# Kernel optimization log

Measured on AMD Instinct MI355X. Metric: run time of the kernel, lower is better.

## Reference

```python
import jax, jax.numpy as jnp
import numpy as np

N, D_IN, D_OUT, E = 8192, 2048, 2048, 8


def setup_inputs() -> dict:
    key = jax.random.key(0)
    k0, k1, k2, k3, k4, k5 = jax.random.split(key, 6)
    s = 1.0 / np.sqrt(D_IN)  # torch nn.Linear default init range
    return {
        "inputs": jax.random.normal(k0, (N, D_IN), jnp.float32),
        "condition": jax.random.normal(k1, (N, D_IN), jnp.float32),
        "Wp": jax.random.uniform(k2, (E, D_IN), jnp.float32, -s, s),
        "bp": jax.random.uniform(k3, (E,), jnp.float32, -s, s),
        "We": jax.random.uniform(k4, (E, D_OUT, D_IN), jnp.float32, -s, s),
        "be": jax.random.uniform(k5, (E, D_OUT), jnp.float32, -s, s),
    }


def reference(inputs, condition, Wp, bp, We, be):
    # predictor: gating logits [N, E]
    prediction = condition @ Wp.T + bp
    # straight-through multiplier: value == 1, gradient flows to prediction
    multiply = jnp.ones_like(prediction) + (prediction - jax.lax.stop_gradient(prediction))
    # run ALL experts on the full batch (faithful to the original): [E, N, F]
    expert_out = jnp.einsum('nd,efd->enf', inputs, We) + be[:, None, :]
    combined = multiply.T[:, :, None] * expert_out  # [E, N, F]
    # select the argmax expert per row
    idx = jnp.argmax(prediction, axis=-1)  # [N]
    result = combined[idx, jnp.arange(prediction.shape[0])]  # [N, F]
    return result
```

## Files before the change

### kernel.cpp

```cpp
#include <hip/hip_runtime.h>
#include <hip/hip_bf16.h>
#include <stdint.h>

#define N_ROWS 8192
#define DIN 2048
#define DOUT 2048
#define NE 8

#define BM3 320
#define BN3 256
#define BK2 64
#define RT3 33
#define NBLK3 (8 * RT3)

#define BM 128
#define BN 128
#define BK 64
#define MAX_RT 71

typedef __bf16 bf16x8 __attribute__((ext_vector_type(8)));
typedef float f32x4 __attribute__((ext_vector_type(4)));

__device__ __forceinline__ uint32_t f2bf(float f) {
  uint32_t u = __builtin_bit_cast(uint32_t, f);
  uint32_t r = u + 0x7FFFu + ((u >> 16) & 1u);
  return r >> 16;
}

__device__ __forceinline__ void gl2lds16(const void* g, void* l) {
  __builtin_amdgcn_global_load_lds(
      (const __attribute__((address_space(1))) unsigned int*)g,
      (__attribute__((address_space(3))) unsigned int*)l, 16, 0, 0);
}

__global__ __launch_bounds__(256) void gate_kernel(
    const float* __restrict__ cond, const float* __restrict__ Wp,
    const float* __restrict__ bp, const float* __restrict__ X,
    int* __restrict__ idx, int* __restrict__ counts, __hip_bfloat16* __restrict__ Xb)
{
  __shared__ int lc[NE];
  const int t = threadIdx.x;
  if (t < NE) lc[t] = 0;

  const int lane = t & 63;
  const int wid  = t >> 6;
  const int row  = blockIdx.x * 4 + wid;

  double acc[NE];
  #pragma unroll
  for (int e = 0; e < NE; ++e) acc[e] = 0.0;

  const float4* crow = (const float4*)(cond + (size_t)row * DIN);
  const float4* wp4  = (const float4*)Wp;
  #pragma unroll
  for (int i = 0; i < DIN / 256; ++i) {
    float4 c = crow[i * 64 + lane];
    #pragma unroll
    for (int e = 0; e < NE; ++e) {
      float4 w = wp4[e * (DIN / 4) + i * 64 + lane];
      acc[e] += (double)c.x * w.x + (double)c.y * w.y
              + (double)c.z * w.z + (double)c.w * w.w;
    }
  }
  #pragma unroll
  for (int e = 0; e < NE; ++e) {
    double v = acc[e];
    #pragma unroll
    for (int off = 32; off > 0; off >>= 1) v += __shfl_down(v, off, 64);
    acc[e] = v;
  }
  __syncthreads();
  if (lane == 0) {
    int best = 0; double bv = acc[0] + (double)bp[0];
    #pragma unroll
    for (int e = 1; e < NE; ++e) {
      double v = acc[e] + (double)bp[e];
      if (v > bv) { bv = v; best = e; }
    }
    idx[row] = best;
    atomicAdd(&lc[best], 1);
  }

  {
    const float4* xs = (const float4*)(X + (size_t)blockIdx.x * 4 * DIN);
    uint4* xd = (uint4*)(Xb + (size_t)blockIdx.x * 4 * DIN);
    #pragma unroll
    for (int c = 0; c < 4; ++c) {
      int ch = t + c * 256;
      float4 v0 = xs[ch * 2];
      float4 v1 = xs[ch * 2 + 1];
      uint4 o;
      o.x = f2bf(v0.x) | (f2bf(v0.y) << 16);
      o.y = f2bf(v0.z) | (f2bf(v0.w) << 16);
      o.z = f2bf(v1.x) | (f2bf(v1.y) << 16);
      o.w = f2bf(v1.z) | (f2bf(v1.w) << 16);
      xd[ch] = o;
    }
  }

  __syncthreads();
  if (t < NE && lc[t] > 0) atomicAdd(&counts[t], lc[t]);
}

__global__ void scan_kernel(const int* __restrict__ counts, int* __restrict__ offsets) {
  if (threadIdx.x == 0 && blockIdx.x == 0) {
    int s = 0;
    for (int e = 0; e < NE; ++e) { offsets[e] = s; s += counts[e]; }
  }
}

__global__ __launch_bounds__(256) void scatter_kernel(
    const int* __restrict__ idx, const int* __restrict__ offsets,
    int* __restrict__ fill, int* __restrict__ rows)
{
  __shared__ int lc[NE], lb[NE];
  const int t = threadIdx.x;
  if (t < NE) lc[t] = 0;
  __syncthreads();
  int n = blockIdx.x * 256 + t;
  int e = idx[n];
  int my = atomicAdd(&lc[e], 1);
  __syncthreads();
  if (t < NE) lb[t] = (lc[t] > 0) ? atomicAdd(&fill[t], lc[t]) : 0;
  __syncthreads();
  rows[offsets[e] + lb[e] + my] = n;
}

__global__ __launch_bounds__(256) void conv_kernel(
    const float* __restrict__ src, __hip_bfloat16* __restrict__ dst, size_t nchunks)
{
  const size_t stride = (size_t)gridDim.x * 256;
  for (size_t c = (size_t)blockIdx.x * 256 + threadIdx.x; c < nchunks; c += stride) {
    float4 v0 = ((const float4*)src)[c * 2];
    float4 v1 = ((const float4*)src)[c * 2 + 1];
    uint4 o;
    o.x = f2bf(v0.x) | (f2bf(v0.y) << 16);
    o.y = f2bf(v0.z) | (f2bf(v0.w) << 16);
    o.z = f2bf(v1.x) | (f2bf(v1.y) << 16);
    o.w = f2bf(v1.z) | (f2bf(v1.w) << 16);
    ((uint4*)dst)[c] = o;
  }
}

__global__ __launch_bounds__(512, 1) void moe_gemm8(
    const __hip_bfloat16* __restrict__ Xb, const __hip_bfloat16* __restrict__ Web,
    const float* __restrict__ be, const int* __restrict__ counts,
    const int* __restrict__ rows, float* __restrict__ out)
{
  __shared__ __align__(16) __hip_bfloat16 Asm[2][2][160 * 64];
  __shared__ __align__(16) __hip_bfloat16 Bsm[2][2][128 * 64];
  __shared__ int rowid[BM3];

  const int bid = blockIdx.x;
  const int w = (bid & 7) * RT3 + (bid >> 3);
  const int ct = w / RT3;
  const int rt = w % RT3;

  int e = 0, racc = 0, cnt = 0, base = 0;
  for (; e < NE; ++e) {
    cnt = counts[e];
    int tiles = (cnt + BM3 - 1) / BM3;
    if (rt < racc + tiles) break;
    racc += tiles; base += cnt;
  }
  if (e == NE) return;
  const int row0 = (rt - racc) * BM3;
  const int tid = threadIdx.x;
  if (tid < BM3)
    rowid[tid] = (row0 + tid < cnt) ? rows[base + row0 + tid] : -1;
  __syncthreads();

  const int lane = tid & 63, wid = tid >> 6;
  const bool w4 = (wid < 4);
  const int wm = wid >> 2, wn = wid & 3;
  const int g = lane >> 4, fr = lane & 15;

  const int cA0 = w4 ? (3 * wid) : (12 + 2 * (wid - 4));
  const int cA1 = cA0 + 1;
  const int cA2 = cA0 + 2;
  const int cB0 = 2 * wid, cB1 = cB0 + 1;

  const int aD0 = cA0 * 1024 + lane * 16;
  const int aD1 = cA1 * 1024 + lane * 16;
  const int aD2 = cA2 * 1024 + lane * 16;
  const int bD0 = cB0 * 1024 + lane * 16;
  const int bD1 = cB1 * 1024 + lane * 16;

  const int frs = lane >> 2, q = lane & 3;
  const __hip_bfloat16 *aP[2][3], *bP[2][2];
  {
    const int cA[3] = {cA0, cA1, cA2};
    const int cB[2] = {cB0, cB1};
    #pragma unroll
    for (int h = 0; h < 2; ++h) {
      #pragma unroll
      for (int s = 0; s < 3; ++s) {
        int c = cA[s];
        int R = h * 160 + (c >> 1) * 16 + frs;
        int gr = rowid[R];
        if (gr < 0) gr = 0;
        aP[h][s] = Xb + (size_t)gr * DIN + (c & 1) * 32 + q * 8;
      }
      #pragma unroll
      for (int s = 0; s < 2; ++s) {
        int c = cB[s];
        size_t wrow = (size_t)e * DOUT + ct * BN3 + h * 128 + (c >> 1) * 16 + frs;
        bP[h][s] = Web + wrow * DIN + (c & 1) * 32 + q * 8;
      }
    }
  }

  f32x4 acc[2][2][5][2];
  #pragma unroll
  for (int a = 0; a < 2; ++a)
    #pragma unroll
    for (int b = 0; b < 2; ++b)
      #pragma unroll
      for (int m = 0; m < 5; ++m)
        #pragma unroll
        for (int n = 0; n < 2; ++n)
          acc[a][b][m][n] = 0.0f;

  bf16x8 av[2][5], bv[2][2];

#define STG_A(buf, h, kel) do {                                              \
    gl2lds16(aP[h][0] + (kel), (char*)&Asm[buf][h][0] + aD0);                \
    gl2lds16(aP[h][1] + (kel), (char*)&Asm[buf][h][0] + aD1);                \
    if (w4) gl2lds16(aP[h][2] + (kel), (char*)&Asm[buf][h][0] + aD2);        \
  } while (0)
#define STG_B(buf, h, kel) do {                                              \
    gl2lds16(bP[h][0] + (kel), (char*)&Bsm[buf][h][0] + bD0);                \
    gl2lds16(bP[h][1] + (kel), (char*)&Bsm[buf][h][0] + bD1); } while (0)

#define READ_A(c, h) do { const char* Ab_ = (const char*)&Asm[c][h][0];      \
    _Pragma("unroll") for (int kk = 0; kk < 2; ++kk)                         \
    _Pragma("unroll") for (int mi = 0; mi < 5; ++mi) {                       \
      int by = (wm * 5 + mi) * 2048 + kk * 1024 + fr * 64 + g * 16;          \
      av[kk][mi] = *(const bf16x8*)(Ab_ + by); } } while (0)

#define READ_B(c, h) do { const char* Bb_ = (const char*)&Bsm[c][h][0];      \
    _Pragma("unroll") for (int kk = 0; kk < 2; ++kk)                         \
    _Pragma("unroll") for (int ni = 0; ni < 2; ++ni) {                       \
      int by = (wn * 2 + ni) * 2048 + kk * 1024 + fr * 64 + g * 16;          \
      bv[kk][ni] = *(const bf16x8*)(Bb_ + by); } } while (0)

#define BAR   __builtin_amdgcn_s_barrier()
#define LGKM0 do { asm volatile("s_waitcnt lgkmcnt(0)" ::: "memory");        \
                   __builtin_amdgcn_sched_barrier(0); } while (0)
#define VMCN  do { if (w4) { asm volatile("s_waitcnt vmcnt(5)" ::: "memory"); } \
                   else    { asm volatile("s_waitcnt vmcnt(4)" ::: "memory"); } \
                   __builtin_amdgcn_sched_barrier(0); } while (0)
#define VMC0  do { asm volatile("s_waitcnt vmcnt(0)" ::: "memory");          \
                   __builtin_amdgcn_sched_barrier(0); } while (0)

#define MFMA_PH(mh, nh) do { __builtin_amdgcn_s_setprio(1);                  \
    _Pragma("unroll") for (int kk = 0; kk < 2; ++kk)                         \
    _Pragma("unroll") for (int mi = 0; mi < 5; ++mi)                         \
    _Pragma("unroll") for (int ni = 0; ni < 2; ++ni)                         \
      acc[mh][nh][mi][ni] = __builtin_amdgcn_mfma_f32_16x16x32_bf16(         \
          av[kk][mi], bv[kk][ni], acc[mh][nh][mi][ni], 0, 0, 0);             \
    __builtin_amdgcn_s_setprio(0); } while (0)

  STG_A(0, 0, 0);  STG_B(0, 0, 0);  STG_A(0, 1, 0);  STG_B(0, 1, 0);
  STG_A(1, 0, 64); STG_B(1, 0, 64);
  VMCN;
  BAR;

  const int T = DIN / BK2;
  #pragma unroll 1
  for (int t = 0; t < T; ++t) {
    const int c = t & 1, o = c ^ 1;
    const int k1 = (t + 1) * BK2, k2 = (t + 2) * BK2;
    const bool s1 = (t + 1 < T), s2 = (t + 2 < T);

    READ_A(c, 0); READ_B(c, 0);
    if (s1) STG_A(o, 1, k1);
    BAR; LGKM0;
    MFMA_PH(0, 0);
    BAR;

    READ_B(c, 1);
    if (s1) STG_B(o, 1, k1);
    BAR; LGKM0;
    MFMA_PH(0, 1);
    BAR;

    READ_A(c, 1); READ_B(c, 0);
    if (s2) STG_A(c, 0, k2);
    BAR; LGKM0;
    MFMA_PH(1, 0);
    BAR;

    READ_B(c, 1);
    if (s2) STG_B(c, 0, k2);
    BAR; LGKM0;
    MFMA_PH(1, 1);
    if (s2) { VMCN; } else { VMC0; }
    BAR;
  }

#undef STG_A
#undef STG_B
#undef READ_A
#undef READ_B
#undef MFMA_PH

  float beh[2][2];
  #pragma unroll
  for (int nh = 0; nh < 2; ++nh)
    #pragma unroll
    for (int ni = 0; ni < 2; ++ni)
      beh[nh][ni] = be[(size_t)e * DOUT + ct * BN3 + nh * 128 + wn * 32 + ni * 16 + fr];

  #pragma unroll
  for (int mh = 0; mh < 2; ++mh)
    #pragma unroll
    for (int mi = 0; mi < 5; ++mi)
      #pragma unroll
      for (int j = 0; j < 4; ++j) {
        int R = mh * 160 + wm * 80 + mi * 16 + g * 4 + j;
        int grow = rowid[R];
        if (grow < 0) continue;
        float* orow = out + (size_t)grow * DOUT + ct * BN3;
        #pragma unroll
        for (int nh = 0; nh < 2; ++nh)
          #pragma unroll
          for (int ni = 0; ni < 2; ++ni)
            orow[nh * 128 + wn * 32 + ni * 16 + fr] = acc[mh][nh][mi][ni][j] + beh[nh][ni];
      }
}

__global__ __launch_bounds__(256) void moe_gemm_fb(
    const float* __restrict__ X, const float* __restrict__ We,
    const float* __restrict__ be, const int* __restrict__ counts,
    const int* __restrict__ offsets, const int* __restrict__ rows,
    float* __restrict__ out)
{
  __shared__ __align__(16) unsigned char Asb[BM * BK * 2];
  __shared__ __align__(16) unsigned char Bsb[BN * BK * 2];
  __shared__ int rowid[BM];

  const int ct = blockIdx.x;
  const int rt = blockIdx.y;

  int e = 0, racc = 0, cnt = 0;
  for (; e < NE; ++e) {
    cnt = counts[e];
    int tiles = (cnt + BM - 1) / BM;
    if (rt < racc + tiles) break;
    racc += tiles;
  }
  if (e == NE) return;
  const int row0 = (rt - racc) * BM;
  const int base = offsets[e];

  if (threadIdx.x < BM) {
    int r = row0 + threadIdx.x;
    rowid[threadIdx.x] = (r < cnt) ? rows[base + r] : -1;
  }
  __syncthreads();

  const int t    = threadIdx.x;
  const int lane = t & 63;
  const int wv   = t >> 6;
  const int wr   = wv >> 1, wc = wv & 1;
  const int g    = lane >> 4, fr = lane & 15;
  const int srow = t >> 4;
  const int skq  = t & 15;

  f32x4 acc[4][4];
  #pragma unroll
  for (int m = 0; m < 4; ++m)
    #pragma unroll
    for (int n = 0; n < 4; ++n)
      acc[m][n] = 0.0f;

  const size_t bcol0 = (size_t)e * DOUT + (size_t)ct * BN;

  for (int k0 = 0; k0 < DIN; k0 += BK) {
    #pragma unroll
    for (int p = 0; p < 8; ++p) {
      int r = p * 16 + srow;
      int gr = rowid[r];
      float4 v = make_float4(0.f, 0.f, 0.f, 0.f);
      if (gr >= 0)
        v = *(const float4*)(X + (size_t)gr * DIN + k0 + skq * 4);
      uint32_t w0 = f2bf(v.x) | (f2bf(v.y) << 16);
      uint32_t w1 = f2bf(v.z) | (f2bf(v.w) << 16);
      int byte = r * (BK * 2) + ((skq * 8) ^ ((r & 7) << 4));
      *(uint2*)(Asb + byte) = make_uint2(w0, w1);
    }
    #pragma unroll
    for (int p = 0; p < 8; ++p) {
      int r = p * 16 + srow;
      float4 v = *(const float4*)(We + (bcol0 + r) * DIN + k0 + skq * 4);
      uint32_t w0 = f2bf(v.x) | (f2bf(v.y) << 16);
      uint32_t w1 = f2bf(v.z) | (f2bf(v.w) << 16);
      int byte = r * (BK * 2) + ((skq * 8) ^ ((r & 7) << 4));
      *(uint2*)(Bsb + byte) = make_uint2(w0, w1);
    }
    __syncthreads();

    #pragma unroll
    for (int kk = 0; kk < BK; kk += 32) {
      bf16x8 av[4], bv[4];
      #pragma unroll
      for (int m = 0; m < 4; ++m) {
        int r = wr * 64 + m * 16 + fr;
        int byte = r * (BK * 2) + ((((kk + g * 8) * 2)) ^ ((r & 7) << 4));
        av[m] = *(const bf16x8*)(Asb + byte);
      }
      #pragma unroll
      for (int n = 0; n < 4; ++n) {
        int c = wc * 64 + n * 16 + fr;
        int byte = c * (BK * 2) + ((((kk + g * 8) * 2)) ^ ((c & 7) << 4));
        bv[n] = *(const bf16x8*)(Bsb + byte);
      }
      #pragma unroll
      for (int m = 0; m < 4; ++m)
        #pragma unroll
        for (int n = 0; n < 4; ++n)
          acc[m][n] = __builtin_amdgcn_mfma_f32_16x16x32_bf16(av[m], bv[n], acc[m][n], 0, 0, 0);
    }
    __syncthreads();
  }

  const float* berow = be + (size_t)e * DOUT + (size_t)ct * BN + wc * 64;
  #pragma unroll
  for (int m = 0; m < 4; ++m) {
    #pragma unroll
    for (int j = 0; j < 4; ++j) {
      int r = wr * 64 + m * 16 + g * 4 + j;
      int grow = rowid[r];
      if (grow < 0) continue;
      float* orow = out + (size_t)grow * DOUT + (size_t)ct * BN + wc * 64;
      #pragma unroll
      for (int n = 0; n < 4; ++n)
        orow[n * 16 + fr] = acc[m][n][j] + berow[n * 16 + fr];
    }
  }
}

extern "C" void kernel_launch(void* const* d_in, const int* in_sizes, int n_in,
                              void* d_out, int out_size, void* d_ws, size_t ws_size,
                              hipStream_t stream) {
  const float* X    = (const float*)d_in[0];
  const float* cond = (const float*)d_in[1];
  const float* Wp   = (const float*)d_in[2];
  const float* bp   = (const float*)d_in[3];
  const float* We   = (const float*)d_in[4];
  const float* be   = (const float*)d_in[5];
  float* out = (float*)d_out;

  int* counts  = (int*)d_ws;
  int* offsets = counts + 8;
  int* fill    = counts + 16;
  int* idx     = (int*)((char*)d_ws + 256);
  int* rows    = idx + N_ROWS;
  const size_t XB_OFF  = 65792;
  const size_t WEB_OFF = XB_OFF + (size_t)N_ROWS * DIN * 2;
  const size_t WS_NEED = WEB_OFF + (size_t)NE * DOUT * DIN * 2;

  hipMemsetAsync(d_ws, 0, 256, stream);

  if (ws_size >= WS_NEED) {
    __hip_bfloat16* Xb  = (__hip_bfloat16*)((char*)d_ws + XB_OFF);
    __hip_bfloat16* Web = (__hip_bfloat16*)((char*)d_ws + WEB_OFF);
    gate_kernel<<<N_ROWS / 4, 256, 0, stream>>>(cond, Wp, bp, X, idx, counts, Xb);
    scan_kernel<<<1, 64, 0, stream>>>(counts, offsets);
    scatter_kernel<<<N_ROWS / 256, 256, 0, stream>>>(idx, offsets, fill, rows);
    conv_kernel<<<2048, 256, 0, stream>>>(We, Web, (size_t)NE * DOUT * DIN / 8);
    moe_gemm8<<<NBLK3, 512, 0, stream>>>(Xb, Web, be, counts, rows, out);
  } else {
    __hip_bfloat16* XbDummy = (__hip_bfloat16*)((char*)d_ws + 256 + 2 * N_ROWS * 4);
    gate_kernel<<<N_ROWS / 4, 256, 0, stream>>>(cond, Wp, bp, X, idx, counts, XbDummy);
    scan_kernel<<<1, 64, 0, stream>>>(counts, offsets);
    scatter_kernel<<<N_ROWS / 256, 256, 0, stream>>>(idx, offsets, fill, rows);
    moe_gemm_fb<<<dim3(DOUT / BN, MAX_RT), 256, 0, stream>>>(X, We, be, counts, offsets, rows, out);
  }
}
```

Measured before the change: 201.8 us.

## Fuse weight conversion into gate kernel; swizzle LDS and restructure GEMM pipeline

Merges the expert-weight fp32-to-bf16 conversion into the gating kernel as extra blocks, which removes one launch and lets the conversion overlap with gating. The GEMM main loop is restructured to prefetch a full K-tile two steps ahead with fewer barriers and partial lgkmcnt waits, interleaving LDS reads with MFMA groups. An XOR swizzle is applied to both the LDS write addresses and the read addresses to reduce bank conflicts. The cost is higher register use from the double A fragments and deeper vmcnt accounting.

After: 532.0 us. +163.6%, slower.

```diff
diff --git a/kernel.cpp b/kernel.cpp
--- a/kernel.cpp
+++ b/kernel.cpp
@@ -13,6 +13,9 @@
 #define RT3 33
 #define NBLK3 (8 * RT3)
 
+#define GATE_BLKS (N_ROWS / 4)
+#define CONV_BLKS 2560
+
 #define BM 128
 #define BN 128
 #define BK 64
@@ -33,13 +36,33 @@
       (__attribute__((address_space(3))) unsigned int*)l, 16, 0, 0);
 }
 
-__global__ __launch_bounds__(256) void gate_kernel(
+__global__ __launch_bounds__(256) void gate_conv_kernel(
     const float* __restrict__ cond, const float* __restrict__ Wp,
     const float* __restrict__ bp, const float* __restrict__ X,
-    int* __restrict__ idx, int* __restrict__ counts, __hip_bfloat16* __restrict__ Xb)
+    const float* __restrict__ We,
+    int* __restrict__ idx, int* __restrict__ counts,
+    __hip_bfloat16* __restrict__ Xb, __hip_bfloat16* __restrict__ Web)
 {
+  const int t = threadIdx.x;
+
+  if (blockIdx.x >= GATE_BLKS) {
+    if (!Web) return;
+    const size_t total = (size_t)NE * DOUT * DIN / 8;
+    const size_t stride = (size_t)CONV_BLKS * 256;
+    for (size_t c = (size_t)(blockIdx.x - GATE_BLKS) * 256 + t; c < total; c += stride) {
+      float4 v0 = ((const float4*)We)[c * 2];
+      float4 v1 = ((const float4*)We)[c * 2 + 1];
+      uint4 o;
+      o.x = f2bf(v0.x) | (f2bf(v0.y) << 16);
+      o.y = f2bf(v0.z) | (f2bf(v0.w) << 16);
+      o.z = f2bf(v1.x) | (f2bf(v1.y) << 16);
+      o.w = f2bf(v1.z) | (f2bf(v1.w) << 16);
+      ((uint4*)Web)[c] = o;
+    }
+    return;
+  }
+
   __shared__ int lc[NE];
-  const int t = threadIdx.x;
   if (t < NE) lc[t] = 0;
 
   const int lane = t & 63;
@@ -81,7 +104,7 @@
     atomicAdd(&lc[best], 1);
   }
 
-  {
+  if (Xb) {
     const float4* xs = (const float4*)(X + (size_t)blockIdx.x * 4 * DIN);
     uint4* xd = (uint4*)(Xb + (size_t)blockIdx.x * 4 * DIN);
     #pragma unroll
@@ -126,22 +149,6 @@
   rows[offsets[e] + lb[e] + my] = n;
 }
 
-__global__ __launch_bounds__(256) void conv_kernel(
-    const float* __restrict__ src, __hip_bfloat16* __restrict__ dst, size_t nchunks)
-{
-  const size_t stride = (size_t)gridDim.x * 256;
-  for (size_t c = (size_t)blockIdx.x * 256 + threadIdx.x; c < nchunks; c += stride) {
-    float4 v0 = ((const float4*)src)[c * 2];
-    float4 v1 = ((const float4*)src)[c * 2 + 1];
-    uint4 o;
-    o.x = f2bf(v0.x) | (f2bf(v0.y) << 16);
-    o.y = f2bf(v0.z) | (f2bf(v0.w) << 16);
-    o.z = f2bf(v1.x) | (f2bf(v1.y) << 16);
-    o.w = f2bf(v1.z) | (f2bf(v1.w) << 16);
-    ((uint4*)dst)[c] = o;
-  }
-}
-
 __global__ __launch_bounds__(512, 1) void moe_gemm8(
     const __hip_bfloat16* __restrict__ Xb, const __hip_bfloat16* __restrict__ Web,
     const float* __restrict__ be, const int* __restrict__ counts,
@@ -174,6 +181,7 @@
   const bool w4 = (wid < 4);
   const int wm = wid >> 2, wn = wid & 3;
   const int g = lane >> 4, fr = lane & 15;
+  const int rsw = fr * 64 + ((g ^ ((fr >> 1) & 3)) << 4);
 
   const int cA0 = w4 ? (3 * wid) : (12 + 2 * (wid - 4));
   const int cA1 = cA0 + 1;
@@ -186,7 +194,8 @@
   const int bD0 = cB0 * 1024 + lane * 16;
   const int bD1 = cB1 * 1024 + lane * 16;
 
-  const int frs = lane >> 2, q = lane & 3;
+  const int frs = lane >> 2;
+  const int qx  = (lane & 3) ^ ((lane >> 3) & 3);
   const __hip_bfloat16 *aP[2][3], *bP[2][2];
   {
     const int cA[3] = {cA0, cA1, cA2};
@@ -199,13 +208,13 @@
         int R = h * 160 + (c >> 1) * 16 + frs;
         int gr = rowid[R];
         if (gr < 0) gr = 0;
-        aP[h][s] = Xb + (size_t)gr * DIN + (c & 1) * 32 + q * 8;
+        aP[h][s] = Xb + (size_t)gr * DIN + (c & 1) * 32 + qx * 8;
       }
       #pragma unroll
       for (int s = 0; s < 2; ++s) {
         int c = cB[s];
         size_t wrow = (size_t)e * DOUT + ct * BN3 + h * 128 + (c >> 1) * 16 + frs;
-        bP[h][s] = Web + wrow * DIN + (c & 1) * 32 + q * 8;
+        bP[h][s] = Web + wrow * DIN + (c & 1) * 32 + qx * 8;
       }
     }
   }
@@ -221,7 +230,7 @@
         for (int n = 0; n < 2; ++n)
           acc[a][b][m][n] = 0.0f;
 
-  bf16x8 av[2][5], bv[2][2];
+  bf16x8 av0[2][5], av1[2][5], bv[2][2][2];
 
 #define STG_A(buf, h, kel) do {                                              \
     gl2lds16(aP[h][0] + (kel), (char*)&Asm[buf][h][0] + aD0);                \
@@ -232,78 +241,68 @@
     gl2lds16(bP[h][0] + (kel), (char*)&Bsm[buf][h][0] + bD0);                \
     gl2lds16(bP[h][1] + (kel), (char*)&Bsm[buf][h][0] + bD1); } while (0)
 
-#define READ_A(c, h) do { const char* Ab_ = (const char*)&Asm[c][h][0];      \
-    _Pragma("unroll") for (int kk = 0; kk < 2; ++kk)                         \
-    _Pragma("unroll") for (int mi = 0; mi < 5; ++mi) {                       \
-      int by = (wm * 5 + mi) * 2048 + kk * 1024 + fr * 64 + g * 16;          \
-      av[kk][mi] = *(const bf16x8*)(Ab_ + by); } } while (0)
-
-#define READ_B(c, h) do { const char* Bb_ = (const char*)&Bsm[c][h][0];      \
-    _Pragma("unroll") for (int kk = 0; kk < 2; ++kk)                         \
-    _Pragma("unroll") for (int ni = 0; ni < 2; ++ni) {                       \
-      int by = (wn * 2 + ni) * 2048 + kk * 1024 + fr * 64 + g * 16;          \
-      bv[kk][ni] = *(const bf16x8*)(Bb_ + by); } } while (0)
+#define RD_A5(dst, cc, h, kk) do { const char* Ab_ = (const char*)&Asm[cc][h][0]; \
+    _Pragma("unroll") for (int mi = 0; mi < 5; ++mi)                         \
+      dst[mi] = *(const bf16x8*)(Ab_ + (wm * 5 + mi) * 2048 + (kk) * 1024 + rsw); } while (0)
+#define RD_B2(cc, h, kk) do { const char* Bb_ = (const char*)&Bsm[cc][h][0]; \
+    _Pragma("unroll") for (int ni = 0; ni < 2; ++ni)                         \
+      bv[h][kk][ni] = *(const bf16x8*)(Bb_ + (wn * 2 + ni) * 2048 + (kk) * 1024 + rsw); } while (0)
 
 #define BAR   __builtin_amdgcn_s_barrier()
-#define LGKM0 do { asm volatile("s_waitcnt lgkmcnt(0)" ::: "memory");        \
-                   __builtin_amdgcn_sched_barrier(0); } while (0)
-#define VMCN  do { if (w4) { asm volatile("s_waitcnt vmcnt(5)" ::: "memory"); } \
-                   else    { asm volatile("s_waitcnt vmcnt(4)" ::: "memory"); } \
+#define SB0   __builtin_amdgcn_sched_barrier(0)
+#define LGKMC(n) do { asm volatile("s_waitcnt lgkmcnt(" #n ")" ::: "memory"); \
+                      __builtin_amdgcn_sched_barrier(0); } while (0)
+#define VMCN  do { if (w4) { asm volatile("s_waitcnt vmcnt(10)" ::: "memory"); } \
+                   else    { asm volatile("s_waitcnt vmcnt(8)"  ::: "memory"); } \
                    __builtin_amdgcn_sched_barrier(0); } while (0)
 #define VMC0  do { asm volatile("s_waitcnt vmcnt(0)" ::: "memory");          \
                    __builtin_amdgcn_sched_barrier(0); } while (0)
 
-#define MFMA_PH(mh, nh) do { __builtin_amdgcn_s_setprio(1);                  \
-    _Pragma("unroll") for (int kk = 0; kk < 2; ++kk)                         \
+#define MF10(avv, kk, mh, nh) do { __builtin_amdgcn_s_setprio(1);            \
     _Pragma("unroll") for (int mi = 0; mi < 5; ++mi)                         \
     _Pragma("unroll") for (int ni = 0; ni < 2; ++ni)                         \
       acc[mh][nh][mi][ni] = __builtin_amdgcn_mfma_f32_16x16x32_bf16(         \
-          av[kk][mi], bv[kk][ni], acc[mh][nh][mi][ni], 0, 0, 0);             \
+          avv[mi], bv[nh][kk][ni], acc[mh][nh][mi][ni], 0, 0, 0);            \
     __builtin_amdgcn_s_setprio(0); } while (0)
 
+#define TILE_BODY(cc, tt_) do {                                              \
+    const int k2_ = ((tt_) + 2) * BK2;                                       \
+    const bool s2_ = ((tt_) + 2 < T);                                        \
+    RD_A5(av0[0], cc, 0, 0); RD_B2(cc, 0, 0); SB0;                    \
+    RD_A5(av0[1], cc, 0, 1); RD_B2(cc, 0, 1); SB0;              \
+    LGKMC(7);  MF10(av0[0], 0, 0, 0);                                        \
+    RD_B2(cc, 1, 0); RD_B2(cc, 1, 1); SB0;                 \
+    LGKMC(4);  MF10(av0[1], 1, 0, 0);                                        \
+    RD_A5(av1[0], cc, 1, 0); RD_A5(av1[1], cc, 1, 1); SB0;    \
+    LGKMC(10); MF10(av0[0], 0, 0, 1); MF10(av0[1], 1, 0, 1);                 \
+    LGKMC(0);  BAR;                                                          \
+    if (s2_) { STG_A(cc, 0, k2_); STG_B(cc, 0, k2_);                         \
+               STG_A(cc, 1, k2_); STG_B(cc, 1, k2_); }                       \
+    MF10(av1[0], 0, 1, 0); MF10(av1[1], 1, 1, 0);                            \
+    MF10(av1[0], 0, 1, 1); MF10(av1[1], 1, 1, 1);                            \
+    if (s2_) { VMCN; } else { VMC0; }                                        \
+    BAR; } while (0)
+
+  const int T = DIN / BK2;
+
   STG_A(0, 0, 0);  STG_B(0, 0, 0);  STG_A(0, 1, 0);  STG_B(0, 1, 0);
-  STG_A(1, 0, 64); STG_B(1, 0, 64);
+  STG_A(1, 0, 64); STG_B(1, 0, 64); STG_A(1, 1, 64); STG_B(1, 1, 64);
   VMCN;
   BAR;
 
-  const int T = DIN / BK2;
   #pragma unroll 1
-  for (int t = 0; t < T; ++t) {
-    const int c = t & 1, o = c ^ 1;
-    const int k1 = (t + 1) * BK2, k2 = (t + 2) * BK2;
-    const bool s1 = (t + 1 < T), s2 = (t + 2 < T);
-
-    READ_A(c, 0); READ_B(c, 0);
-    if (s1) STG_A(o, 1, k1);
-    BAR; LGKM0;
-    MFMA_PH(0, 0);
-    BAR;
-
-    READ_B(c, 1);
-    if (s1) STG_B(o, 1, k1);
-    BAR; LGKM0;
-    MFMA_PH(0, 1);
-    BAR;
-
-    READ_A(c, 1); READ_B(c, 0);
-    if (s2) STG_A(c, 0, k2);
-    BAR; LGKM0;
-    MFMA_PH(1, 0);
-    BAR;
-
-    READ_B(c, 1);
-    if (s2) STG_B(c, 0, k2);
-    BAR; LGKM0;
-    MFMA_PH(1, 1);
-    if (s2) { VMCN; } else { VMC0; }
-    BAR;
+  for (int tt = 0; tt < T / 2; ++tt) {
+    const int t2 = tt * 2;
+    TILE_BODY(0, t2);
+    TILE_BODY(1, t2 + 1);
   }
 
 #undef STG_A
 #undef STG_B
-#undef READ_A
-#undef READ_B
-#undef MFMA_PH
+#undef RD_A5
+#undef RD_B2
+#undef MF10
+#undef TILE_BODY
 
   float beh[2][2];
   #pragma unroll
@@ -466,14 +465,14 @@
   if (ws_size >= WS_NEED) {
     __hip_bfloat16* Xb  = (__hip_bfloat16*)((char*)d_ws + XB_OFF);
     __hip_bfloat16* Web = (__hip_bfloat16*)((char*)d_ws + WEB_OFF);
-    gate_kernel<<<N_ROWS / 4, 256, 0, stream>>>(cond, Wp, bp, X, idx, counts, Xb);
+    gate_conv_kernel<<<GATE_BLKS + CONV_BLKS, 256, 0, stream>>>(
+        cond, Wp, bp, X, We, idx, counts, Xb, Web);
     scan_kernel<<<1, 64, 0, stream>>>(counts, offsets);
     scatter_kernel<<<N_ROWS / 256, 256, 0, stream>>>(idx, offsets, fill, rows);
-    conv_kernel<<<2048, 256, 0, stream>>>(We, Web, (size_t)NE * DOUT * DIN / 8);
     moe_gemm8<<<NBLK3, 512, 0, stream>>>(Xb, Web, be, counts, rows, out);
   } else {
-    __hip_bfloat16* XbDummy = (__hip_bfloat16*)((char*)d_ws + 256 + 2 * N_ROWS * 4);
-    gate_kernel<<<N_ROWS / 4, 256, 0, stream>>>(cond, Wp, bp, X, idx, counts, XbDummy);
+    gate_conv_kernel<<<GATE_BLKS + CONV_BLKS, 256, 0, stream>>>(
+        cond, Wp, bp, X, We, idx, counts, nullptr, nullptr);
     scan_kernel<<<1, 64, 0, stream>>>(counts, offsets);
     scatter_kernel<<<N_ROWS / 256, 256, 0, stream>>>(idx, offsets, fill, rows);
     moe_gemm_fb<<<dim3(DOUT / BN, MAX_RT), 256, 0, stream>>>(X, We, be, counts, offsets, rows, out);
```
